# Kernel optimization log

Hardware: AMD Instinct MI355X
Metric: run time of the kernel (lower is better)

## Reference

```python
import jax, jax.numpy as jnp
import numpy as np

N_NODES = 100000
N_EDGES = 1600000  # random edges; self-loops appended -> 1.7M total
NFEATS, NHIDS, NCLASSES = 512, 256, 40


def _spmm(edge_row, edge_col, edge_val, dense):
    # out[r] += val * dense[c]  (COO spmm)
    msgs = edge_val[:, None] * dense[edge_col]           # [E, F]
    return jax.ops.segment_sum(msgs, edge_row, num_segments=N_NODES)


def setup_inputs() -> dict:
    key = jax.random.key(0)
    ks = jax.random.split(key, 8)
    x = jax.random.normal(ks[0], (N_NODES, NFEATS), dtype=jnp.float32)
    stdv1 = 1.0 / np.sqrt(NHIDS)
    W1 = jax.random.uniform(ks[1], (NFEATS, NHIDS), minval=-stdv1, maxval=stdv1, dtype=jnp.float32)
    b1 = jax.random.uniform(ks[2], (NHIDS,), minval=-stdv1, maxval=stdv1, dtype=jnp.float32)
    stdv2 = 1.0 / np.sqrt(NCLASSES)
    W2 = jax.random.uniform(ks[3], (NHIDS, NCLASSES), minval=-stdv2, maxval=stdv2, dtype=jnp.float32)
    b2 = jax.random.uniform(ks[4], (NCLASSES,), minval=-stdv2, maxval=stdv2, dtype=jnp.float32)

    # random adjacency edges + self-loops (normalized_adj does adj = I + adj)
    r = jax.random.randint(ks[5], (N_EDGES,), 0, N_NODES, dtype=jnp.int32)
    c = jax.random.randint(ks[6], (N_EDGES,), 0, N_NODES, dtype=jnp.int32)
    sl = jnp.arange(N_NODES, dtype=jnp.int32)
    edge_row = jnp.concatenate([r, sl])
    edge_col = jnp.concatenate([c, sl])
    raw_val = jnp.ones(edge_row.shape[0], dtype=jnp.float32)
    # deg = row-sum of (A + I); symmetric normalization D^-1/2 (A+I) D^-1/2
    deg = jax.ops.segment_sum(raw_val, edge_row, num_segments=N_NODES)
    dinv = jnp.power(deg, -0.5)
    dinv = jnp.where(jnp.isfinite(dinv), dinv, 0.0)
    edge_val = dinv[edge_row] * raw_val * dinv[edge_col]
    return {"x": x, "W1": W1, "b1": b1, "W2": W2, "b2": b2,
            "edge_row": edge_row, "edge_col": edge_col, "edge_val": edge_val}


def reference(x, W1, b1, W2, b2, edge_row, edge_col, edge_val):
    # layer 1: relu(spmm(adj, x@W1) + b1); dropout skipped (eval mode)
    h = jax.nn.relu(_spmm(edge_row, edge_col, edge_val, x @ W1) + b1)
    # layer 2: spmm(adj, h@W2) + b2
    out = _spmm(edge_row, edge_col, edge_val, h @ W2) + b2
    return out
```

## Files before the change

### kernel.cpp

```cpp
#include <hip/hip_runtime.h>
#include <hip/hip_bf16.h>


#define NFEATS 512
#define NHIDS  256
#define NCLS   40
#define NCLSP  64

typedef unsigned short ushort_t;
typedef unsigned int uint_t;
typedef __attribute__((ext_vector_type(8))) short frag8;
typedef __attribute__((ext_vector_type(4))) float floatx4;

#define AS1C(p) ((__attribute__((address_space(1))) const void*)(p))
#define AS3(p)  ((__attribute__((address_space(3))) void*)(p))

__device__ __forceinline__ ushort_t f2b(float f) {
    uint_t u = __float_as_uint(f);
    uint_t r = (u + 0x7fffu + ((u >> 16) & 1u)) >> 16;
    return (ushort_t)r;
}
__device__ __forceinline__ float b2f(ushort_t b) {
    return __uint_as_float((uint_t)b << 16);
}


__global__ void hist_kernel(const int* __restrict__ row, int* __restrict__ cnt, int E) {
    int e = blockIdx.x * blockDim.x + threadIdx.x;
    if (e < E) atomicAdd(&cnt[row[e]], 1);
}

#define PS_T 256
#define PS_C 4
#define PS_CHUNK (PS_T * PS_C)

__global__ __launch_bounds__(PS_T) void scan_partial_kernel(const int* __restrict__ cnt,
                                                            int* __restrict__ blockSums, int N) {
    __shared__ int sm[PS_T];
    int t = threadIdx.x;
    int base = blockIdx.x * PS_CHUNK + t * PS_C;
    int s = 0;
    if (base + PS_C <= N) {
        int4 v = *(const int4*)(cnt + base);
        s = v.x + v.y + v.z + v.w;
    } else {
        for (int i = 0; i < PS_C; i++) if (base + i < N) s += cnt[base + i];
    }
    sm[t] = s;
    __syncthreads();
    for (int off = PS_T / 2; off > 0; off >>= 1) {
        if (t < off) sm[t] += sm[t + off];
        __syncthreads();
    }
    if (t == 0) blockSums[blockIdx.x] = sm[0];
}

#define SS_T 128
__global__ __launch_bounds__(SS_T) void scan_sums_kernel(int* __restrict__ blockSums, int B) {
    __shared__ int sm[SS_T];
    int t = threadIdx.x;
    int v = (t < B) ? blockSums[t] : 0;
    sm[t] = v;
    __syncthreads();
    for (int off = 1; off < SS_T; off <<= 1) {
        int x = (t >= off) ? sm[t - off] : 0;
        __syncthreads();
        sm[t] += x;
        __syncthreads();
    }
    if (t < B) blockSums[t] = sm[t] - v;
}

__global__ __launch_bounds__(PS_T) void scan_finalize_kernel(int* __restrict__ cnt,
                                                             const int* __restrict__ blockSums,
                                                             int* __restrict__ row_ptr, int N, int E) {
    __shared__ int sm[PS_T];
    int t = threadIdx.x;
    int base = blockIdx.x * PS_CHUNK + t * PS_C;
    int vals[PS_C];
    int s = 0;
#pragma unroll
    for (int i = 0; i < PS_C; i++) {
        int idx = base + i;
        vals[i] = (idx < N) ? cnt[idx] : 0;
        s += vals[i];
    }
    sm[t] = s;
    __syncthreads();
    for (int off = 1; off < PS_T; off <<= 1) {
        int x = (t >= off) ? sm[t - off] : 0;
        __syncthreads();
        sm[t] += x;
        __syncthreads();
    }
    int run = blockSums[blockIdx.x] + sm[t] - s;
#pragma unroll
    for (int i = 0; i < PS_C; i++) {
        int idx = base + i;
        if (idx < N) {
            row_ptr[idx] = run;
            run += vals[i];
            cnt[idx] = 0;
        }
    }
    if (blockIdx.x == 0 && t == 0) row_ptr[N] = E;
}

__global__ void scatter_kernel(const int* __restrict__ row, const int* __restrict__ col,
                               const float* __restrict__ val, const int* __restrict__ row_ptr,
                               int* __restrict__ fill, int2* __restrict__ cv, int E) {
    int e = blockIdx.x * blockDim.x + threadIdx.x;
    if (e < E) {
        int r = row[e];
        int p = row_ptr[r] + atomicAdd(&fill[r], 1);
        cv[p] = make_int2(col[e], __float_as_int(val[e]));
    }
}


__global__ void convert_w1(const float* __restrict__ W1, ushort_t* __restrict__ W1f) {
    int idx = blockIdx.x * 256 + threadIdx.x;
    int j    = idx & 7;
    int lane = (idx >> 3) & 63;
    int nt   = (idx >> 9) & 3;
    int t    = (idx >> 11) & 15;
    int nb   = idx >> 15;
    int n = nb * 64 + nt * 16 + (lane & 15);
    int k = t * 32 + (lane >> 4) * 8 + j;
    W1f[idx] = f2b(W1[k * NHIDS + n]);
}

__global__ void convert_w2(const float* __restrict__ W2, ushort_t* __restrict__ W2f) {
    int idx = blockIdx.x * 256 + threadIdx.x;
    int j    = idx & 7;
    int lane = (idx >> 3) & 63;
    int nt   = (idx >> 9) & 3;
    int s    = idx >> 11;
    int n = nt * 16 + (lane & 15);
    int k = s * 32 + (lane >> 4) * 8 + j;
    W2f[idx] = (n < NCLS) ? f2b(W2[k * NCLS + n]) : (ushort_t)0;
}


#define G1_BM 64
#define G1_BK 32

__global__ __launch_bounds__(256) void gemm1_kernel(const float* __restrict__ A,
                                                    const ushort_t* __restrict__ W1f,
                                                    ushort_t* __restrict__ H1, int M) {
    __shared__ float As[2][G1_BM * G1_BK];
    int tid  = threadIdx.x;
    int wave = tid >> 6, lane = tid & 63;
    int quad = lane >> 4, ln = lane & 15;
    int m0 = blockIdx.x * G1_BM;

    int rloc0 = (wave * 2 + 0) * 8 + (lane >> 3);
    int rloc1 = (wave * 2 + 1) * 8 + (lane >> 3);
    int sslot = (lane & 7) ^ ((lane >> 3) & 7);
    int gr0 = m0 + rloc0; if (gr0 > M - 1) gr0 = M - 1;
    int gr1 = m0 + rloc1; if (gr1 > M - 1) gr1 = M - 1;
    const float* src0 = A + (size_t)gr0 * NFEATS + sslot * 4;
    const float* src1 = A + (size_t)gr1 * NFEATS + sslot * 4;
    float* dst0 = &As[0][(wave * 2 + 0) * 256];
    float* dst1 = &As[0][(wave * 2 + 1) * 256];
    float* dst0b = &As[1][(wave * 2 + 0) * 256];
    float* dst1b = &As[1][(wave * 2 + 1) * 256];

    const ushort_t* bbase = W1f + (size_t)(wave * 16) * 2048 + lane * 8;

    floatx4 acc[4][4] = {};

    __builtin_amdgcn_global_load_lds(AS1C(src0), AS3(dst0), 16, 0, 0);
    __builtin_amdgcn_global_load_lds(AS1C(src1), AS3(dst1), 16, 0, 0);
    __syncthreads();

#pragma unroll 2
    for (int t = 0; t < NFEATS / G1_BK; ++t) {
        int cur = t & 1;
        if (t < NFEATS / G1_BK - 1) {
            const float* s0 = src0 + (t + 1) * G1_BK;
            const float* s1 = src1 + (t + 1) * G1_BK;
            if (cur == 0) {
                __builtin_amdgcn_global_load_lds(AS1C(s0), AS3(dst0b), 16, 0, 0);
                __builtin_amdgcn_global_load_lds(AS1C(s1), AS3(dst1b), 16, 0, 0);
            } else {
                __builtin_amdgcn_global_load_lds(AS1C(s0), AS3(dst0), 16, 0, 0);
                __builtin_amdgcn_global_load_lds(AS1C(s1), AS3(dst1), 16, 0, 0);
            }
        }
        frag8 bfr[4], af[4];
        const ushort_t* bstep = bbase + (size_t)t * 2048;
#pragma unroll
        for (int nt = 0; nt < 4; nt++)
            bfr[nt] = *(const frag8*)(bstep + nt * 512);
#pragma unroll
        for (int mt = 0; mt < 4; mt++) {
            int R = mt * 16 + ln;
            int sw = R & 7;
            const float* base = &As[cur][R * G1_BK];
            float4 lo = *(const float4*)(base + (((2 * quad)     ^ sw) * 4));
            float4 hi = *(const float4*)(base + (((2 * quad + 1) ^ sw) * 4));
            union { frag8 f; uint_t u[4]; } fu;
            asm volatile("v_cvt_pk_bf16_f32 %0, %1, %2" : "=v"(fu.u[0]) : "v"(lo.x), "v"(lo.y));
            asm volatile("v_cvt_pk_bf16_f32 %0, %1, %2" : "=v"(fu.u[1]) : "v"(lo.z), "v"(lo.w));
            asm volatile("v_cvt_pk_bf16_f32 %0, %1, %2" : "=v"(fu.u[2]) : "v"(hi.x), "v"(hi.y));
            asm volatile("v_cvt_pk_bf16_f32 %0, %1, %2" : "=v"(fu.u[3]) : "v"(hi.z), "v"(hi.w));
            af[mt] = fu.f;
        }
#pragma unroll
        for (int mt = 0; mt < 4; mt++)
#pragma unroll
            for (int nt = 0; nt < 4; nt++)
                acc[mt][nt] = __builtin_amdgcn_mfma_f32_16x16x32_bf16(af[mt], bfr[nt], acc[mt][nt], 0, 0, 0);
        __syncthreads();
    }

#pragma unroll
    for (int mt = 0; mt < 4; mt++) {
#pragma unroll
        for (int i = 0; i < 4; i++) {
            int m = m0 + mt * 16 + quad * 4 + i;
            if (m < M) {
#pragma unroll
                for (int nt = 0; nt < 4; nt++) {
                    H1[(size_t)m * NHIDS + wave * 64 + nt * 16 + ln] = f2b(acc[mt][nt][i]);
                }
            }
        }
    }
}


__global__ __launch_bounds__(256) void spmm1_kernel(const int* __restrict__ row_ptr,
                                                    const int2* __restrict__ cv,
                                                    const ushort_t* __restrict__ H1,
                                                    const float* __restrict__ b1,
                                                    ushort_t* __restrict__ AGG, int N) {
    int wave = threadIdx.x >> 6, lane = threadIdx.x & 63;
    int r = blockIdx.x * 4 + wave;
    if (r >= N) return;
    int s = row_ptr[r], e = row_ptr[r + 1];
    float a0 = 0.f, a1 = 0.f, a2 = 0.f, a3 = 0.f;
    int j = s;
    for (; j + 3 < e; j += 4) {
        int2 p0 = cv[j];
        int2 p1 = cv[j + 1];
        int2 p2 = cv[j + 2];
        int2 p3 = cv[j + 3];
        ushort4 h0 = *(const ushort4*)(H1 + (size_t)p0.x * NHIDS + lane * 4);
        ushort4 h1 = *(const ushort4*)(H1 + (size_t)p1.x * NHIDS + lane * 4);
        ushort4 h2 = *(const ushort4*)(H1 + (size_t)p2.x * NHIDS + lane * 4);
        ushort4 h3 = *(const ushort4*)(H1 + (size_t)p3.x * NHIDS + lane * 4);
        float v0 = __int_as_float(p0.y), v1 = __int_as_float(p1.y);
        float v2 = __int_as_float(p2.y), v3 = __int_as_float(p3.y);
        a0 += v0 * b2f(h0.x); a1 += v0 * b2f(h0.y); a2 += v0 * b2f(h0.z); a3 += v0 * b2f(h0.w);
        a0 += v1 * b2f(h1.x); a1 += v1 * b2f(h1.y); a2 += v1 * b2f(h1.z); a3 += v1 * b2f(h1.w);
        a0 += v2 * b2f(h2.x); a1 += v2 * b2f(h2.y); a2 += v2 * b2f(h2.z); a3 += v2 * b2f(h2.w);
        a0 += v3 * b2f(h3.x); a1 += v3 * b2f(h3.y); a2 += v3 * b2f(h3.z); a3 += v3 * b2f(h3.w);
    }
    for (; j < e; j++) {
        int2 p0 = cv[j];
        ushort4 h0 = *(const ushort4*)(H1 + (size_t)p0.x * NHIDS + lane * 4);
        float v0 = __int_as_float(p0.y);
        a0 += v0 * b2f(h0.x); a1 += v0 * b2f(h0.y); a2 += v0 * b2f(h0.z); a3 += v0 * b2f(h0.w);
    }
    float4 bb = *(const float4*)(b1 + lane * 4);
    a0 += bb.x; a1 += bb.y; a2 += bb.z; a3 += bb.w;
    ushort4 o;
    o.x = f2b(a0 > 0.f ? a0 : 0.f);
    o.y = f2b(a1 > 0.f ? a1 : 0.f);
    o.z = f2b(a2 > 0.f ? a2 : 0.f);
    o.w = f2b(a3 > 0.f ? a3 : 0.f);
    *(ushort4*)&AGG[(size_t)r * NHIDS + lane * 4] = o;
}


__global__ __launch_bounds__(256) void gemm2_kernel(const ushort_t* __restrict__ AGG,
                                                    const ushort_t* __restrict__ W2f,
                                                    ushort_t* __restrict__ H2, int M) {
    int tid  = threadIdx.x;
    int wave = tid >> 6, lane = tid & 63;
    int quad = lane >> 4, ln = lane & 15;
    int m0 = blockIdx.x * 256 + wave * 64;

    floatx4 acc[4][4] = {};
    frag8 zf = {};

#pragma unroll
    for (int s = 0; s < NHIDS / 32; s++) {
        int k0 = s * 32;
        frag8 af[4], bf[4];
#pragma unroll
        for (int mt = 0; mt < 4; mt++) {
            int m = m0 + mt * 16 + ln;
            af[mt] = (m < M) ? *(const frag8*)(AGG + (size_t)m * NHIDS + k0 + quad * 8) : zf;
        }
#pragma unroll
        for (int nt = 0; nt < 4; nt++)
            bf[nt] = *(const frag8*)(W2f + (size_t)(s * 4 + nt) * 512 + lane * 8);
#pragma unroll
        for (int mt = 0; mt < 4; mt++)
#pragma unroll
            for (int nt = 0; nt < 4; nt++)
                acc[mt][nt] = __builtin_amdgcn_mfma_f32_16x16x32_bf16(af[mt], bf[nt], acc[mt][nt], 0, 0, 0);
    }
#pragma unroll
    for (int mt = 0; mt < 4; mt++) {
#pragma unroll
        for (int i = 0; i < 4; i++) {
            int m = m0 + mt * 16 + quad * 4 + i;
            if (m < M) {
#pragma unroll
                for (int nt = 0; nt < 4; nt++)
                    H2[(size_t)m * NCLSP + nt * 16 + ln] = f2b(acc[mt][nt][i]);
            }
        }
    }
}


__global__ __launch_bounds__(256) void spmm2_kernel(const int* __restrict__ row_ptr,
                                                    const int2* __restrict__ cv,
                                                    const ushort_t* __restrict__ H2,
                                                    const float* __restrict__ b2,
                                                    float* __restrict__ out, int N) {
    int wave = threadIdx.x >> 6, lane = threadIdx.x & 63;
    int half = lane >> 5, fl = lane & 31;
    int r = blockIdx.x * 8 + wave * 2 + half;
    if (r >= N) return;
    int s = row_ptr[r], e = row_ptr[r + 1];
    float a0 = 0.f, a1 = 0.f;
    int j = s;
    for (; j + 3 < e; j += 4) {
        int2 p0 = cv[j];
        int2 p1 = cv[j + 1];
        int2 p2 = cv[j + 2];
        int2 p3 = cv[j + 3];
        float v0 = __int_as_float(p0.y);
        float v1 = __int_as_float(p1.y);
        float v2 = __int_as_float(p2.y);
        float v3 = __int_as_float(p3.y);
        uint_t h0 = *(const uint_t*)(H2 + (size_t)p0.x * NCLSP + fl * 2);
        uint_t h1 = *(const uint_t*)(H2 + (size_t)p1.x * NCLSP + fl * 2);
        uint_t h2 = *(const uint_t*)(H2 + (size_t)p2.x * NCLSP + fl * 2);
        uint_t h3 = *(const uint_t*)(H2 + (size_t)p3.x * NCLSP + fl * 2);
        a0 += v0 * b2f((ushort_t)(h0 & 0xffff));
        a1 += v0 * b2f((ushort_t)(h0 >> 16));
        a0 += v1 * b2f((ushort_t)(h1 & 0xffff));
        a1 += v1 * b2f((ushort_t)(h1 >> 16));
        a0 += v2 * b2f((ushort_t)(h2 & 0xffff));
        a1 += v2 * b2f((ushort_t)(h2 >> 16));
        a0 += v3 * b2f((ushort_t)(h3 & 0xffff));
        a1 += v3 * b2f((ushort_t)(h3 >> 16));
    }
    for (; j < e; j++) {
        int2 p = cv[j];
        float v = __int_as_float(p.y);
        uint_t h = *(const uint_t*)(H2 + (size_t)p.x * NCLSP + fl * 2);
        a0 += v * b2f((ushort_t)(h & 0xffff));
        a1 += v * b2f((ushort_t)(h >> 16));
    }
    if (fl < NCLS / 2) {
        float2 o;
        o.x = a0 + b2[fl * 2];
        o.y = a1 + b2[fl * 2 + 1];
        *(float2*)(out + (size_t)r * NCLS + fl * 2) = o;
    }
}


static inline size_t align256(size_t x) { return (x + 255) & ~(size_t)255; }

extern "C" void kernel_launch(void* const* d_in, const int* in_sizes, int n_in,
                              void* d_out, int out_size, void* d_ws, size_t ws_size,
                              hipStream_t stream) {
    const float* x        = (const float*)d_in[0];
    const float* W1       = (const float*)d_in[1];
    const float* b1       = (const float*)d_in[2];
    const float* W2       = (const float*)d_in[3];
    const float* b2       = (const float*)d_in[4];
    const int*   edge_row = (const int*)d_in[5];
    const int*   edge_col = (const int*)d_in[6];
    const float* edge_val = (const float*)d_in[7];
    float* out = (float*)d_out;

    int N = in_sizes[0] / NFEATS;
    int E = in_sizes[5];

    char* w = (char*)d_ws;
    size_t off = 0;
    ushort_t* H1   = (ushort_t*)(w + off); off += align256((size_t)N * NHIDS * 2);
    ushort_t* AGG  = (ushort_t*)(w + off); off += align256((size_t)N * NHIDS * 2);
    ushort_t* H2   = (ushort_t*)(w + off); off += align256((size_t)N * NCLSP * 2);
    ushort_t* W1f  = (ushort_t*)(w + off); off += align256((size_t)NHIDS * NFEATS * 2);
    ushort_t* W2f  = (ushort_t*)(w + off); off += align256((size_t)NCLSP * NHIDS * 2);
    int*      row_ptr = (int*)(w + off); off += align256((size_t)(N + 1) * 4);
    int*      cnt     = (int*)(w + off); off += align256((size_t)N * 4);
    int*      blockSums = (int*)(w + off); off += align256((size_t)SS_T * 4);
    int2*     cv      = (int2*)(w + off); off += align256((size_t)E * 8);

    int scanB = (N + PS_CHUNK - 1) / PS_CHUNK;

    hipMemsetAsync(cnt, 0, (size_t)N * 4, stream);
    hist_kernel<<<(E + 255) / 256, 256, 0, stream>>>(edge_row, cnt, E);
    convert_w1<<<(NFEATS * NHIDS) / 256, 256, 0, stream>>>(W1, W1f);
    convert_w2<<<(NCLSP * NHIDS) / 256, 256, 0, stream>>>(W2, W2f);
    scan_partial_kernel<<<scanB, PS_T, 0, stream>>>(cnt, blockSums, N);
    scan_sums_kernel<<<1, SS_T, 0, stream>>>(blockSums, scanB);
    scan_finalize_kernel<<<scanB, PS_T, 0, stream>>>(cnt, blockSums, row_ptr, N, E);
    scatter_kernel<<<(E + 255) / 256, 256, 0, stream>>>(edge_row, edge_col, edge_val,
                                                        row_ptr, cnt, cv, E);

    gemm1_kernel<<<(N + G1_BM - 1) / G1_BM, 256, 0, stream>>>(x, W1f, H1, N);
    spmm1_kernel<<<(N + 3) / 4, 256, 0, stream>>>(row_ptr, cv, H1, b1, AGG, N);

    gemm2_kernel<<<(N + 255) / 256, 256, 0, stream>>>(AGG, W2f, H2, N);
    spmm2_kernel<<<(N + 7) / 8, 256, 0, stream>>>(row_ptr, cv, H2, b2, out, N);
}
```

Before: 671.0 us.

## Deepen gemm1 LDS pipeline to four stages and shrink H2 row stride to 40

The gemm1 kernel now uses a 4-stage LDS ring buffer. It prefetches three K-tiles ahead with global_load_lds, double-buffers the W1 fragments in registers, and replaces __syncthreads with a raw s_barrier plus a manual vmcnt wait, so memory latency overlaps with MFMA work. Separately, H2 is stored unpadded with 40 columns instead of 64. gemm2 drops the fourth N-tile and spmm2 gathers from the narrower rows, which cuts gather traffic. The hand-tuned waitcnt and barrier scheduling risks races if the vmcnt accounting is wrong.

```diff
diff --git a/kernel.cpp b/kernel.cpp
--- a/kernel.cpp
+++ b/kernel.cpp
@@ -5,7 +5,6 @@
 #define NFEATS 512
 #define NHIDS  256
 #define NCLS   40
-#define NCLSP  64
 
 typedef unsigned short ushort_t;
 typedef unsigned int uint_t;
@@ -148,7 +147,7 @@
 __global__ __launch_bounds__(256) void gemm1_kernel(const float* __restrict__ A,
                                                     const ushort_t* __restrict__ W1f,
                                                     ushort_t* __restrict__ H1, int M) {
-    __shared__ float As[2][G1_BM * G1_BK];
+    __shared__ float As[4][G1_BM * G1_BK];
     int tid  = threadIdx.x;
     int wave = tid >> 6, lane = tid & 63;
     int quad = lane >> 4, ln = lane & 15;
@@ -161,43 +160,45 @@
     int gr1 = m0 + rloc1; if (gr1 > M - 1) gr1 = M - 1;
     const float* src0 = A + (size_t)gr0 * NFEATS + sslot * 4;
     const float* src1 = A + (size_t)gr1 * NFEATS + sslot * 4;
-    float* dst0 = &As[0][(wave * 2 + 0) * 256];
-    float* dst1 = &As[0][(wave * 2 + 1) * 256];
-    float* dst0b = &As[1][(wave * 2 + 0) * 256];
-    float* dst1b = &As[1][(wave * 2 + 1) * 256];
 
     const ushort_t* bbase = W1f + (size_t)(wave * 16) * 2048 + lane * 8;
 
     floatx4 acc[4][4] = {};
-
-    __builtin_amdgcn_global_load_lds(AS1C(src0), AS3(dst0), 16, 0, 0);
-    __builtin_amdgcn_global_load_lds(AS1C(src1), AS3(dst1), 16, 0, 0);
-    __syncthreads();
-
-#pragma unroll 2
+    frag8 bfrA[4], bfrB[4];
+
+#define G1_STAGE(t) do { \
+        float* d0_ = &As[(t) & 3][(wave * 2 + 0) * 256]; \
+        float* d1_ = &As[(t) & 3][(wave * 2 + 1) * 256]; \
+        __builtin_amdgcn_global_load_lds(AS1C(src0 + (t) * G1_BK), AS3(d0_), 16, 0, 0); \
+        __builtin_amdgcn_global_load_lds(AS1C(src1 + (t) * G1_BK), AS3(d1_), 16, 0, 0); \
+    } while (0)
+
+#define G1_LOADB(t, dst) do { \
+        const ushort_t* bs_ = bbase + (size_t)(t) * 2048; \
+        dst[0] = *(const frag8*)(bs_); \
+        dst[1] = *(const frag8*)(bs_ + 512); \
+        dst[2] = *(const frag8*)(bs_ + 1024); \
+        dst[3] = *(const frag8*)(bs_ + 1536); \
+    } while (0)
+
+    G1_STAGE(0);
+    G1_STAGE(1);
+    G1_LOADB(0, bfrA);
+    G1_STAGE(2);
+    G1_LOADB(1, bfrB);
+    asm volatile("s_waitcnt vmcnt(12)" ::: "memory");
+    __builtin_amdgcn_sched_barrier(0);
+
+#pragma unroll
     for (int t = 0; t < NFEATS / G1_BK; ++t) {
-        int cur = t & 1;
-        if (t < NFEATS / G1_BK - 1) {
-            const float* s0 = src0 + (t + 1) * G1_BK;
-            const float* s1 = src1 + (t + 1) * G1_BK;
-            if (cur == 0) {
-                __builtin_amdgcn_global_load_lds(AS1C(s0), AS3(dst0b), 16, 0, 0);
-                __builtin_amdgcn_global_load_lds(AS1C(s1), AS3(dst1b), 16, 0, 0);
-            } else {
-                __builtin_amdgcn_global_load_lds(AS1C(s0), AS3(dst0), 16, 0, 0);
-                __builtin_amdgcn_global_load_lds(AS1C(s1), AS3(dst1), 16, 0, 0);
-            }
-        }
-        frag8 bfr[4], af[4];
-        const ushort_t* bstep = bbase + (size_t)t * 2048;
-#pragma unroll
-        for (int nt = 0; nt < 4; nt++)
-            bfr[nt] = *(const frag8*)(bstep + nt * 512);
+        __builtin_amdgcn_s_barrier();
+        __builtin_amdgcn_sched_barrier(0);
+        frag8 af[4];
 #pragma unroll
         for (int mt = 0; mt < 4; mt++) {
             int R = mt * 16 + ln;
             int sw = R & 7;
-            const float* base = &As[cur][R * G1_BK];
+            const float* base = &As[t & 3][R * G1_BK];
             float4 lo = *(const float4*)(base + (((2 * quad)     ^ sw) * 4));
             float4 hi = *(const float4*)(base + (((2 * quad + 1) ^ sw) * 4));
             union { frag8 f; uint_t u[4]; } fu;
@@ -207,12 +208,23 @@
             asm volatile("v_cvt_pk_bf16_f32 %0, %1, %2" : "=v"(fu.u[3]) : "v"(hi.z), "v"(hi.w));
             af[mt] = fu.f;
         }
-#pragma unroll
-        for (int mt = 0; mt < 4; mt++)
-#pragma unroll
-            for (int nt = 0; nt < 4; nt++)
-                acc[mt][nt] = __builtin_amdgcn_mfma_f32_16x16x32_bf16(af[mt], bfr[nt], acc[mt][nt], 0, 0, 0);
-        __syncthreads();
+        if (t < 13) G1_STAGE(t + 3);
+        __builtin_amdgcn_sched_barrier(0);
+        if ((t & 1) == 0) {
+#pragma unroll
+            for (int mt = 0; mt < 4; mt++)
+#pragma unroll
+                for (int nt = 0; nt < 4; nt++)
+                    acc[mt][nt] = __builtin_amdgcn_mfma_f32_16x16x32_bf16(af[mt], bfrA[nt], acc[mt][nt], 0, 0, 0);
+            if (t < 14) G1_LOADB(t + 2, bfrA);
+        } else {
+#pragma unroll
+            for (int mt = 0; mt < 4; mt++)
+#pragma unroll
+                for (int nt = 0; nt < 4; nt++)
+                    acc[mt][nt] = __builtin_amdgcn_mfma_f32_16x16x32_bf16(af[mt], bfrB[nt], acc[mt][nt], 0, 0, 0);
+            if (t < 14) G1_LOADB(t + 2, bfrB);
+        }
     }
 
 #pragma unroll
@@ -228,6 +240,8 @@
             }
         }
     }
+#undef G1_STAGE
+#undef G1_LOADB
 }
 
 
@@ -283,25 +297,25 @@
     int quad = lane >> 4, ln = lane & 15;
     int m0 = blockIdx.x * 256 + wave * 64;
 
-    floatx4 acc[4][4] = {};
+    floatx4 acc[4][3] = {};
     frag8 zf = {};
 
 #pragma unroll
     for (int s = 0; s < NHIDS / 32; s++) {
         int k0 = s * 32;
-        frag8 af[4], bf[4];
+        frag8 af[4], bf[3];
 #pragma unroll
         for (int mt = 0; mt < 4; mt++) {
             int m = m0 + mt * 16 + ln;
             af[mt] = (m < M) ? *(const frag8*)(AGG + (size_t)m * NHIDS + k0 + quad * 8) : zf;
         }
 #pragma unroll
-        for (int nt = 0; nt < 4; nt++)
+        for (int nt = 0; nt < 3; nt++)
             bf[nt] = *(const frag8*)(W2f + (size_t)(s * 4 + nt) * 512 + lane * 8);
 #pragma unroll
         for (int mt = 0; mt < 4; mt++)
 #pragma unroll
-            for (int nt = 0; nt < 4; nt++)
+            for (int nt = 0; nt < 3; nt++)
                 acc[mt][nt] = __builtin_amdgcn_mfma_f32_16x16x32_bf16(af[mt], bf[nt], acc[mt][nt], 0, 0, 0);
     }
 #pragma unroll
@@ -310,9 +324,10 @@
         for (int i = 0; i < 4; i++) {
             int m = m0 + mt * 16 + quad * 4 + i;
             if (m < M) {
-#pragma unroll
-                for (int nt = 0; nt < 4; nt++)
-                    H2[(size_t)m * NCLSP + nt * 16 + ln] = f2b(acc[mt][nt][i]);
+                H2[(size_t)m * NCLS + ln]      = f2b(acc[mt][0][i]);
+                H2[(size_t)m * NCLS + 16 + ln] = f2b(acc[mt][1][i]);
+                if (ln < 8)
+                    H2[(size_t)m * NCLS + 32 + ln] = f2b(acc[mt][2][i]);
             }
         }
     }
@@ -327,7 +342,7 @@
     int wave = threadIdx.x >> 6, lane = threadIdx.x & 63;
     int half = lane >> 5, fl = lane & 31;
     int r = blockIdx.x * 8 + wave * 2 + half;
-    if (r >= N) return;
+    if (r >= N || fl >= NCLS / 2) return;
     int s = row_ptr[r], e = row_ptr[r + 1];
     float a0 = 0.f, a1 = 0.f;
     int j = s;
@@ -340,10 +355,10 @@
         float v1 = __int_as_float(p1.y);
         float v2 = __int_as_float(p2.y);
         float v3 = __int_as_float(p3.y);
-        uint_t h0 = *(const uint_t*)(H2 + (size_t)p0.x * NCLSP + fl * 2);
-        uint_t h1 = *(const uint_t*)(H2 + (size_t)p1.x * NCLSP + fl * 2);
-        uint_t h2 = *(const uint_t*)(H2 + (size_t)p2.x * NCLSP + fl * 2);
-        uint_t h3 = *(const uint_t*)(H2 + (size_t)p3.x * NCLSP + fl * 2);
+        uint_t h0 = *(const uint_t*)(H2 + (size_t)p0.x * NCLS + fl * 2);
+        uint_t h1 = *(const uint_t*)(H2 + (size_t)p1.x * NCLS + fl * 2);
+        uint_t h2 = *(const uint_t*)(H2 + (size_t)p2.x * NCLS + fl * 2);
+        uint_t h3 = *(const uint_t*)(H2 + (size_t)p3.x * NCLS + fl * 2);
         a0 += v0 * b2f((ushort_t)(h0 & 0xffff));
         a1 += v0 * b2f((ushort_t)(h0 >> 16));
         a0 += v1 * b2f((ushort_t)(h1 & 0xffff));
@@ -356,16 +371,14 @@
     for (; j < e; j++) {
         int2 p = cv[j];
         float v = __int_as_float(p.y);
-        uint_t h = *(const uint_t*)(H2 + (size_t)p.x * NCLSP + fl * 2);
+        uint_t h = *(const uint_t*)(H2 + (size_t)p.x * NCLS + fl * 2);
         a0 += v * b2f((ushort_t)(h & 0xffff));
         a1 += v * b2f((ushort_t)(h >> 16));
     }
-    if (fl < NCLS / 2) {
-        float2 o;
-        o.x = a0 + b2[fl * 2];
-        o.y = a1 + b2[fl * 2 + 1];
-        *(float2*)(out + (size_t)r * NCLS + fl * 2) = o;
-    }
+    float2 o;
+    o.x = a0 + b2[fl * 2];
+    o.y = a1 + b2[fl * 2 + 1];
+    *(float2*)(out + (size_t)r * NCLS + fl * 2) = o;
 }
 
 
@@ -391,9 +404,9 @@
     size_t off = 0;
     ushort_t* H1   = (ushort_t*)(w + off); off += align256((size_t)N * NHIDS * 2);
     ushort_t* AGG  = (ushort_t*)(w + off); off += align256((size_t)N * NHIDS * 2);
-    ushort_t* H2   = (ushort_t*)(w + off); off += align256((size_t)N * NCLSP * 2);
+    ushort_t* H2   = (ushort_t*)(w + off); off += align256((size_t)N * NCLS * 2);
     ushort_t* W1f  = (ushort_t*)(w + off); off += align256((size_t)NHIDS * NFEATS * 2);
-    ushort_t* W2f  = (ushort_t*)(w + off); off += align256((size_t)NCLSP * NHIDS * 2);
+    ushort_t* W2f  = (ushort_t*)(w + off); off += align256((size_t)64 * NHIDS * 2);
     int*      row_ptr = (int*)(w + off); off += align256((size_t)(N + 1) * 4);
     int*      cnt     = (int*)(w + off); off += align256((size_t)N * 4);
     int*      blockSums = (int*)(w + off); off += align256((size_t)SS_T * 4);
@@ -404,7 +417,7 @@
     hipMemsetAsync(cnt, 0, (size_t)N * 4, stream);
     hist_kernel<<<(E + 255) / 256, 256, 0, stream>>>(edge_row, cnt, E);
     convert_w1<<<(NFEATS * NHIDS) / 256, 256, 0, stream>>>(W1, W1f);
-    convert_w2<<<(NCLSP * NHIDS) / 256, 256, 0, stream>>>(W2, W2f);
+    convert_w2<<<(64 * NHIDS) / 256, 256, 0, stream>>>(W2, W2f);
     scan_partial_kernel<<<scanB, PS_T, 0, stream>>>(cnt, blockSums, N);
     scan_sums_kernel<<<1, SS_T, 0, stream>>>(blockSums, scanB);
     scan_finalize_kernel<<<scanB, PS_T, 0, stream>>>(cnt, blockSums, row_ptr, N, E);
```

New measurement: 665.5 us. About the same (-0.8%).
